# Optimization experiments

Measured on AMD Instinct MI355X. Metric: run time of the kernel, lower is better.

## Reference

```python
import jax, jax.numpy as jnp
import numpy as np
from jax.scipy.special import erf

L = 10          # grid_num_levels = int(log(8192/16)/log(2)) + 1
D = 4           # grid_level_dim
T = 1 << 21     # hash table size per level (2**log2_hashmap_size)
BASE = 16
RES = (BASE * (2 ** np.arange(L))).astype(np.float32)   # [16 .. 8192]
PRIMES = np.array([1, 2654435761, 805459861], dtype=np.uint32)
DIM_DIR_ENC = 3 + 2 * 3 * 4   # 27


def contract_mean_std(x, std):
    # mip-nerf-360 scene contraction + std scaled by |det J|^(1/3)
    r2 = jnp.maximum(jnp.sum(x * x, -1, keepdims=True), 1e-8)
    r = jnp.sqrt(r2)
    f = (2.0 * r - 1.0) / r2                  # tangential Jacobian eigenvalue
    z = jnp.where(r2 <= 1.0, x, f * x)
    det = (f * f) * (1.0 / r2)                # two tangential * one radial (1/r^2)
    scale = jnp.where(r2[..., 0] <= 1.0, 1.0, det[..., 0] ** (1.0 / 3.0))
    return z, std * scale


def pos_enc(x, min_deg=0, max_deg=4):
    scales = 2.0 ** jnp.arange(min_deg, max_deg, dtype=jnp.float32)
    xb = (x[..., None, :] * scales[:, None]).reshape(x.shape[:-1] + (-1,))
    four = jnp.sin(jnp.concatenate([xb, xb + 0.5 * jnp.pi], -1))
    return jnp.concatenate([x, four], -1)     # [..., 27]


def hash_grid_encode(x01, table):
    # x01: [..., 3] in [0,1]; table: [L, T, D] -> features [..., L, D]
    res = jnp.asarray(RES)
    primes = jnp.asarray(PRIMES)
    pos = x01[..., None, :] * res[:, None]    # [..., L, 3]
    pf = jnp.floor(pos)
    frac = pos - pf                           # differentiable w.r.t. pos
    base = pf.astype(jnp.uint32)
    lvl = jnp.arange(L)
    out = jnp.zeros(x01.shape[:-1] + (L, D), x01.dtype)
    for c in range(8):                        # fixed 8 trilinear corners
        off = np.array([(c >> 0) & 1, (c >> 1) & 1, (c >> 2) & 1], np.uint32)
        h = (base + off) * primes             # uint32 wraps = spatial hash
        idx = ((h[..., 0] ^ h[..., 1] ^ h[..., 2]) & jnp.uint32(T - 1)).astype(jnp.int32)
        w = jnp.prod(jnp.where(off.astype(bool), frac, 1.0 - frac), axis=-1)  # [..., L]
        out = out + w[..., None] * table[lvl, idx]   # irregular gather [..., L, D]
    return out


def reference(means, stds, viewdirs, table, W1, b1, W2, b2, Wd0, bd0, Wd1, bd1, Wrgb, brgb):
    # predict_density: warp_fn='contract', then bound=2 rescale
    m, s = contract_mean_std(means, stds)
    m, s = m / 2.0, s / 2.0
    x01 = (m + 1.0) / 2.0                     # encoder bound=1 -> [0,1]
    feats = hash_grid_encode(x01, table)      # [R, S, n, L, D]
    aw = erf(1.0 / jnp.sqrt(8.0 * (s[..., None] ** 2) * (jnp.asarray(RES) ** 2)))  # [R,S,n,L]
    feats = jnp.mean(feats * aw[..., None], axis=-3)        # mean over gaussian samples n
    feats = feats.reshape(feats.shape[:-2] + (L * D,))      # [R, S, 40]
    x = jax.nn.relu(feats @ W1 + b1) @ W2 + b2              # density MLP -> [R, S, 256]
    density = jax.nn.softplus(x[..., 0] - 1.0)              # density_bias = -1
    de = pos_enc(viewdirs)                                  # [R, 27]
    de = jnp.broadcast_to(de[..., None, :], x.shape[:-1] + (de.shape[-1],))
    inp = jnp.concatenate([x, de], -1)                      # [R, S, 283]
    y = jax.nn.relu(inp @ Wd0 + bd0)
    y = jnp.concatenate([y, inp], -1)                       # skip_layer_dir = 0
    y = jax.nn.relu(y @ Wd1 + bd1)
    rgb = jax.nn.sigmoid(y @ Wrgb + brgb)                   # premult=1, bias=0
    rgb = rgb * (1.0 + 2.0 * 0.001) - 0.001                 # rgb_padding
    return jnp.concatenate([density[..., None], rgb], -1)   # [R, S, 4] = (density, rgb)


def _linear(key, fan_in, fan_out):
    kw, kb = jax.random.split(key)
    s = 1.0 / np.sqrt(fan_in)
    W = jax.random.uniform(kw, (fan_in, fan_out), jnp.float32, -s, s)
    b = jax.random.uniform(kb, (fan_out,), jnp.float32, -s, s)
    return W, b


def setup_inputs() -> dict:
    key = jax.random.key(0)
    ks = jax.random.split(key, 10)
    R_, S_, n_ = 4096, 32, 6
    means = jax.random.normal(ks[0], (R_, S_, n_, 3), jnp.float32) * 1.5
    stds = jax.random.uniform(ks[1], (R_, S_, n_), jnp.float32) * 0.2 + 0.01
    vd = jax.random.normal(ks[2], (R_, 3), jnp.float32)
    viewdirs = vd / jnp.linalg.norm(vd, axis=-1, keepdims=True)
    table = jax.random.uniform(ks[3], (L, T, D), jnp.float32, -1e-4, 1e-4)
    W1, b1 = _linear(ks[4], L * D, 64)
    W2, b2 = _linear(ks[5], 64, 256)
    Wd0, bd0 = _linear(ks[6], 256 + DIM_DIR_ENC, 256)
    Wd1, bd1 = _linear(ks[7], 256 + 256 + DIM_DIR_ENC, 256)
    Wrgb, brgb = _linear(ks[8], 256, 3)
    return dict(means=means, stds=stds, viewdirs=viewdirs, table=table,
                W1=W1, b1=b1, W2=W2, b2=b2, Wd0=Wd0, bd0=bd0,
                Wd1=Wd1, bd1=bd1, Wrgb=Wrgb, brgb=brgb)
```

## Files before the change

kernel.cpp:

```cpp
#include <hip/hip_runtime.h>
#include <hip/hip_bf16.h>
#include <math.h>
#include <string.h>

#define NR 4096
#define NSMP 32
#define NG 6
#define NP (NR*NSMP)
#define NPS (NP*NG)
#define NL 10
#define TBL (1u<<21)
#define TMASK (TBL-1u)
#define PR1 2654435761u
#define PR2 805459861u

typedef __hip_bfloat16 bf16;
typedef __attribute__((ext_vector_type(8))) short short8;
typedef __attribute__((ext_vector_type(4))) float f32x4;

__device__ inline short f2bf_bits(float f) {
    __hip_bfloat16 h = __float2bfloat16(f);
    return (short)__builtin_bit_cast(unsigned short, h);
}

__global__ __launch_bounds__(256) void k_contract(const float* __restrict__ means,
                                                  const float* __restrict__ stds,
                                                  float4* __restrict__ ctr) {
    int i = blockIdx.x * 256 + threadIdx.x;
    if (i >= NPS) return;
    float x = means[i*3+0], y = means[i*3+1], z = means[i*3+2];
    float r2 = fmaxf(x*x + y*y + z*z, 1e-8f);
    float r  = sqrtf(r2);
    float f  = (2.f*r - 1.f) / r2;
    float zx, zy, zz, scale;
    if (r2 <= 1.f) { zx = x; zy = y; zz = z; scale = 1.f; }
    else { zx = f*x; zy = f*y; zz = f*z; scale = cbrtf(f*f / r2); }
    float s = stds[i] * scale * 0.5f;
    ctr[i] = make_float4(zx*0.25f + 0.5f, zy*0.25f + 0.5f, zz*0.25f + 0.5f, s);
}

__global__ __launch_bounds__(256) void k_encode(const float4* __restrict__ ctr,
                                                const float* __restrict__ table,
                                                float4* __restrict__ feats) {
    int p = blockIdx.x * 256 + threadIdx.x;
    int l = blockIdx.y;
    float res = (float)(16 << l);
    const float* tl = table + (size_t)l * TBL * 4u;
    float a0 = 0.f, a1 = 0.f, a2 = 0.f, a3 = 0.f;
    for (int s = 0; s < NG; s++) {
        float4 c = ctr[p*NG + s];
        float sr = c.w * res;
        float aw = erff(rsqrtf(8.f * sr * sr));
        float px = c.x*res, py = c.y*res, pz = c.z*res;
        float fx = floorf(px), fy = floorf(py), fz = floorf(pz);
        float rx = px - fx, ry = py - fy, rz = pz - fz;
        unsigned bx = (unsigned)fx, by = (unsigned)fy, bz = (unsigned)fz;
        unsigned hx[2] = { bx, bx + 1u };
        unsigned hy[2] = { by * PR1, (by + 1u) * PR1 };
        unsigned hz[2] = { bz * PR2, (bz + 1u) * PR2 };
        float wx[2] = { 1.f - rx, rx };
        float wy[2] = { 1.f - ry, ry };
        float wz[2] = { 1.f - rz, rz };
        #pragma unroll
        for (int cz = 0; cz < 2; cz++)
        #pragma unroll
        for (int cy = 0; cy < 2; cy++)
        #pragma unroll
        for (int cx = 0; cx < 2; cx++) {
            unsigned idx = (hx[cx] ^ hy[cy] ^ hz[cz]) & TMASK;
            float4 fv = *(const float4*)(tl + (size_t)idx * 4u);
            float w = wx[cx] * wy[cy] * wz[cz] * aw;
            a0 += w * fv.x; a1 += w * fv.y; a2 += w * fv.z; a3 += w * fv.w;
        }
    }
    const float inv = 1.f / 6.f;
    feats[(size_t)p * NL + l] = make_float4(a0*inv, a1*inv, a2*inv, a3*inv);
}

__global__ void k_dirs(const float* __restrict__ vd, float* __restrict__ de) {
    int r = blockIdx.x * 64 + threadIdx.x;
    if (r >= NR) return;
    float v0 = vd[r*3], v1 = vd[r*3+1], v2 = vd[r*3+2];
    float* o = de + r * 27;
    o[0] = v0; o[1] = v1; o[2] = v2;
    float v[3] = { v0, v1, v2 };
    #pragma unroll
    for (int sc = 0; sc < 4; sc++) {
        float scale = (float)(1 << sc);
        #pragma unroll
        for (int d = 0; d < 3; d++) {
            float xb = v[d] * scale;
            o[3  + sc*3 + d] = sinf(xb);
            o[15 + sc*3 + d] = cosf(xb);
        }
    }
}

__global__ __launch_bounds__(256) void k_l1(const float* __restrict__ Af,
                                            const float* __restrict__ W,
                                            const float* __restrict__ bias,
                                            bf16* __restrict__ Cout) {
    const int K = 40, N = 64;
    __shared__ float As[16][68];
    __shared__ float Ws[16][64];
    int tid = threadIdx.x;
    int tx = tid & 15, ty = tid >> 4;
    int m0 = blockIdx.x * 64;
    float acc[4][4] = {};
    for (int kb = 0; kb < K; kb += 16) {
        #pragma unroll
        for (int i = 0; i < 4; i++) {
            int idx = tid + i * 256;
            int kk = idx & 15, mm = idx >> 4;
            int k = kb + kk;
            As[kk][mm] = (k < K) ? Af[(size_t)(m0 + mm) * 40 + k] : 0.f;
        }
        #pragma unroll
        for (int i = 0; i < 4; i++) {
            int idx = tid + i * 256;
            int c = idx & 63, rr = idx >> 6;
            int k = kb + rr;
            Ws[rr][c] = (k < K) ? W[(size_t)k * N + c] : 0.f;
        }
        __syncthreads();
        #pragma unroll
        for (int kk = 0; kk < 16; kk++) {
            float4 a = *(const float4*)&As[kk][ty * 4];
            float4 b = *(const float4*)&Ws[kk][tx * 4];
            float av[4] = { a.x, a.y, a.z, a.w };
            float bv[4] = { b.x, b.y, b.z, b.w };
            #pragma unroll
            for (int i2 = 0; i2 < 4; i2++)
            #pragma unroll
            for (int j = 0; j < 4; j++)
                acc[i2][j] += av[i2] * bv[j];
        }
        __syncthreads();
    }
    #pragma unroll
    for (int i = 0; i < 4; i++) {
        int m = m0 + ty * 4 + i;
        #pragma unroll
        for (int j = 0; j < 4; j++) {
            int n = tx * 4 + j;
            float v = fmaxf(acc[i][j] + bias[n], 0.f);
            Cout[(size_t)m * N + n] = __float2bfloat16(v);
        }
    }
}

__global__ __launch_bounds__(256) void k_prepw(const float* __restrict__ W2,
                                               const float* __restrict__ Wd0,
                                               const float* __restrict__ Wd1,
                                               short* __restrict__ Wt2,
                                               short* __restrict__ Wt3,
                                               short* __restrict__ Wt4) {
    int i = blockIdx.x * 256 + threadIdx.x;
    if (i < 256*64) {
        int n = i >> 6, k = i & 63;
        Wt2[i] = f2bf_bits(W2[(size_t)k*256 + n]);
        return;
    }
    i -= 256*64;
    if (i < 256*320) {
        int n = i / 320, k = i % 320;
        Wt3[i] = f2bf_bits(k < 283 ? Wd0[(size_t)k*256 + n] : 0.f);
        return;
    }
    i -= 256*320;
    if (i < 256*576) {
        int n = i / 576, k = i % 576;
        Wt4[i] = f2bf_bits(k < 539 ? Wd1[(size_t)k*256 + n] : 0.f);
    }
}

template<int LAYER>
__device__ inline short8 load_chunk(const short* __restrict__ A0,
                                    const short* __restrict__ A1,
                                    const float* __restrict__ de,
                                    int m, int k) {
    if constexpr (LAYER == 2) {
        return *(const short8*)(A0 + (size_t)m * 64 + k);
    } else if constexpr (LAYER == 3) {
        if (k < 256) return *(const short8*)(A0 + (size_t)m * 256 + k);
        short8 v;
        int ray = m >> 5;
        #pragma unroll
        for (int j = 0; j < 8; j++) {
            int kk = k + j - 256;
            v[j] = f2bf_bits((kk < 27) ? de[ray * 27 + kk] : 0.f);
        }
        return v;
    } else {
        if (k < 256) return *(const short8*)(A0 + (size_t)m * 256 + k);
        if (k < 512) return *(const short8*)(A1 + (size_t)m * 256 + (k - 256));
        short8 v;
        int ray = m >> 5;
        #pragma unroll
        for (int j = 0; j < 8; j++) {
            int kk = k + j - 512;
            v[j] = f2bf_bits((kk < 27) ? de[ray * 27 + kk] : 0.f);
        }
        return v;
    }
}

template<int LAYER>
__global__ __launch_bounds__(256) void k_mlp(const short* __restrict__ A0,
                                             const short* __restrict__ A1,
                                             const float* __restrict__ de,
                                             const short* __restrict__ Wt,
                                             const float* __restrict__ bias,
                                             short* __restrict__ Cout,
                                             float* __restrict__ dens) {
    constexpr int KP = (LAYER == 2) ? 64 : (LAYER == 3) ? 320 : 576;
    __shared__ __align__(16) char As[8192];
    int tid = threadIdx.x;
    int wid = tid >> 6, lane = tid & 63;
    int m0 = blockIdx.x * 64;
    int l15 = lane & 15, l4 = lane >> 4;

    f32x4 acc[4][4] = {};
    for (int kt = 0; kt < KP / 64; kt++) {
        #pragma unroll
        for (int i = 0; i < 2; i++) {
            int q = tid + i * 256;
            int m = q >> 3, k8 = q & 7;
            short8 v = load_chunk<LAYER>(A0, A1, de, m0 + m, kt * 64 + k8 * 8);
            *(short8*)(As + ((m * 128 + k8 * 16) ^ ((m & 7) << 4))) = v;
        }
        __syncthreads();
        #pragma unroll
        for (int ks = 0; ks < 2; ks++) {
            short8 bfr[4], afr[4];
            #pragma unroll
            for (int nf = 0; nf < 4; nf++)
                bfr[nf] = *(const short8*)(Wt + (size_t)(wid * 64 + nf * 16 + l15) * KP
                                              + kt * 64 + ks * 32 + l4 * 8);
            #pragma unroll
            for (int mf = 0; mf < 4; mf++) {
                int m = mf * 16 + l15;
                afr[mf] = *(const short8*)(As + ((m * 128 + (ks * 4 + l4) * 16) ^ ((m & 7) << 4)));
            }
            #pragma unroll
            for (int mf = 0; mf < 4; mf++)
            #pragma unroll
            for (int nf = 0; nf < 4; nf++)
                acc[mf][nf] = __builtin_amdgcn_mfma_f32_16x16x32_bf16(afr[mf], bfr[nf], acc[mf][nf], 0, 0, 0);
        }
        __syncthreads();
    }

    #pragma unroll
    for (int mf = 0; mf < 4; mf++) {
        #pragma unroll
        for (int nf = 0; nf < 4; nf++) {
            int col = wid * 64 + nf * 16 + l15;
            float b = bias[col];
            #pragma unroll
            for (int r = 0; r < 4; r++) {
                int row = m0 + mf * 16 + l4 * 4 + r;
                float v = acc[mf][nf][r] + b;
                if constexpr (LAYER == 2) {
                    if (col == 0) {
                        float t = v - 1.f;
                        dens[(size_t)row * 4] = (t > 20.f) ? t : log1pf(expf(t));
                    }
                } else {
                    v = fmaxf(v, 0.f);
                }
                Cout[(size_t)row * 256 + col] = f2bf_bits(v);
            }
        }
    }
}

__global__ __launch_bounds__(256) void k_rgb(const short* __restrict__ y1,
                                             const float* __restrict__ Wrgb,
                                             const float* __restrict__ brgb,
                                             float* __restrict__ out) {
    typedef __attribute__((ext_vector_type(4))) short short4v;
    int lane = threadIdx.x & 63;
    int p = blockIdx.x * 4 + (threadIdx.x >> 6);
    short4v yv = *(const short4v*)(y1 + (size_t)p * 256 + lane * 4);
    float y[4];
    #pragma unroll
    for (int j = 0; j < 4; j++) {
        unsigned u = ((unsigned)(unsigned short)yv[j]) << 16;
        y[j] = __builtin_bit_cast(float, u);
    }
    float4 w0 = *(const float4*)(Wrgb + lane * 12);
    float4 w1 = *(const float4*)(Wrgb + lane * 12 + 4);
    float4 w2 = *(const float4*)(Wrgb + lane * 12 + 8);
    float wf[12] = { w0.x, w0.y, w0.z, w0.w, w1.x, w1.y, w1.z, w1.w, w2.x, w2.y, w2.z, w2.w };
    float a0 = 0.f, a1 = 0.f, a2 = 0.f;
    #pragma unroll
    for (int j = 0; j < 4; j++) {
        a0 += y[j] * wf[j*3 + 0];
        a1 += y[j] * wf[j*3 + 1];
        a2 += y[j] * wf[j*3 + 2];
    }
    #pragma unroll
    for (int off = 32; off > 0; off >>= 1) {
        a0 += __shfl_xor(a0, off);
        a1 += __shfl_xor(a1, off);
        a2 += __shfl_xor(a2, off);
    }
    if (lane == 0) {
        float s0 = 1.f / (1.f + expf(-(a0 + brgb[0])));
        float s1 = 1.f / (1.f + expf(-(a1 + brgb[1])));
        float s2 = 1.f / (1.f + expf(-(a2 + brgb[2])));
        out[(size_t)p * 4 + 1] = s0 * 1.002f - 0.001f;
        out[(size_t)p * 4 + 2] = s1 * 1.002f - 0.001f;
        out[(size_t)p * 4 + 3] = s2 * 1.002f - 0.001f;
    }
}

extern "C" void kernel_launch(void* const* d_in, const int* in_sizes, int n_in,
                              void* d_out, int out_size, void* d_ws, size_t ws_size,
                              hipStream_t stream) {
    const float* means = (const float*)d_in[0];
    const float* stds  = (const float*)d_in[1];
    const float* vd    = (const float*)d_in[2];
    const float* table = (const float*)d_in[3];
    const float* W1    = (const float*)d_in[4];
    const float* b1    = (const float*)d_in[5];
    const float* W2    = (const float*)d_in[6];
    const float* b2    = (const float*)d_in[7];
    const float* Wd0   = (const float*)d_in[8];
    const float* bd0   = (const float*)d_in[9];
    const float* Wd1   = (const float*)d_in[10];
    const float* bd1   = (const float*)d_in[11];
    const float* Wrgb  = (const float*)d_in[12];
    const float* brgb  = (const float*)d_in[13];
    float* out = (float*)d_out;

    char* ws = (char*)d_ws;
    float4* ctr   = (float4*)(ws);
    float4* feats = (float4*)(ws + 12582912);
    float*  de    = (float*) (ws + 33554432);
    short*  h1    = (short*) (ws + 33996800);
    short*  x     = (short*) (ws + 50774016);
    short*  y0    = (short*) (ws + 117882880);
    short*  y1    = (short*) (ws + 184991744);
    short*  Wt2   = (short*)(ws);
    short*  Wt3   = (short*)(ws + 32768);
    short*  Wt4   = (short*)(ws + 196608);

    k_contract<<<dim3(NPS/256), 256, 0, stream>>>(means, stds, ctr);
    k_encode<<<dim3(NP/256, NL), 256, 0, stream>>>(ctr, table, feats);
    k_dirs<<<dim3(NR/64), 64, 0, stream>>>(vd, de);
    k_prepw<<<dim3(960), 256, 0, stream>>>(W2, Wd0, Wd1, Wt2, Wt3, Wt4);
    k_l1<<<dim3(NP/64), 256, 0, stream>>>((const float*)feats, W1, b1, (bf16*)h1);
    k_mlp<2><<<dim3(NP/64), 256, 0, stream>>>(h1, nullptr, nullptr, Wt2, b2, x, out);
    k_mlp<3><<<dim3(NP/64), 256, 0, stream>>>(x, nullptr, de, Wt3, bd0, y0, nullptr);
    k_mlp<4><<<dim3(NP/64), 256, 0, stream>>>(y0, x, de, Wt4, bd1, y1, nullptr);
    k_rgb<<<dim3(NP/4), 256, 0, stream>>>(y1, Wrgb, brgb, out);
}
```

Measured before the change: 1.164 ms.

## Gather hash grid levels 3+ from a bf16 copy of the table

Adds a pre-pass that converts hash-table levels 3 through 9 to bf16 in workspace, then splits the encoder into a float path for coarse levels and a bf16 path for fine levels. The aim is to halve the bytes fetched per random corner gather and improve cache residency for the large levels. This adds a full-table conversion pass each call and reduces the precision of the table features; the sample loop is also unrolled.

Measured after the change: 1.147 ms. No clear change (-1.5%).

```diff
diff --git a/kernel.cpp b/kernel.cpp
--- a/kernel.cpp
+++ b/kernel.cpp
@@ -13,6 +13,8 @@
 #define TMASK (TBL-1u)
 #define PR1 2654435761u
 #define PR2 805459861u
+#define HLV0 3
+#define NHL (NL - HLV0)
 
 typedef __hip_bfloat16 bf16;
 typedef __attribute__((ext_vector_type(8))) short short8;
@@ -21,6 +23,9 @@
 __device__ inline short f2bf_bits(float f) {
     __hip_bfloat16 h = __float2bfloat16(f);
     return (short)__builtin_bit_cast(unsigned short, h);
+}
+__device__ inline float bfbits2f(unsigned short u) {
+    return __builtin_bit_cast(float, ((unsigned)u) << 16);
 }
 
 __global__ __launch_bounds__(256) void k_contract(const float* __restrict__ means,
@@ -39,14 +44,34 @@
     ctr[i] = make_float4(zx*0.25f + 0.5f, zy*0.25f + 0.5f, zz*0.25f + 0.5f, s);
 }
 
+__global__ __launch_bounds__(256) void k_prept(const float* __restrict__ table,
+                                               ushort4* __restrict__ th) {
+    size_t i = ((size_t)blockIdx.x * 256 + threadIdx.x) * 2;
+    const float4* src = (const float4*)(table + (size_t)HLV0 * TBL * 4u);
+    #pragma unroll
+    for (int j = 0; j < 2; j++) {
+        float4 v = src[i + j];
+        ushort4 o;
+        o.x = (unsigned short)f2bf_bits(v.x);
+        o.y = (unsigned short)f2bf_bits(v.y);
+        o.z = (unsigned short)f2bf_bits(v.z);
+        o.w = (unsigned short)f2bf_bits(v.w);
+        th[i + j] = o;
+    }
+}
+
+template<int BASE, bool HI>
 __global__ __launch_bounds__(256) void k_encode(const float4* __restrict__ ctr,
                                                 const float* __restrict__ table,
+                                                const ushort4* __restrict__ th,
                                                 float4* __restrict__ feats) {
     int p = blockIdx.x * 256 + threadIdx.x;
-    int l = blockIdx.y;
+    int l = BASE + blockIdx.y;
     float res = (float)(16 << l);
-    const float* tl = table + (size_t)l * TBL * 4u;
+    const float4* tf = (const float4*)(table + (size_t)l * TBL * 4u);
+    const ushort4* thl = th + (size_t)(l - HLV0) * TBL;
     float a0 = 0.f, a1 = 0.f, a2 = 0.f, a3 = 0.f;
+    #pragma unroll
     for (int s = 0; s < NG; s++) {
         float4 c = ctr[p*NG + s];
         float sr = c.w * res;
@@ -68,9 +93,17 @@
         #pragma unroll
         for (int cx = 0; cx < 2; cx++) {
             unsigned idx = (hx[cx] ^ hy[cy] ^ hz[cz]) & TMASK;
-            float4 fv = *(const float4*)(tl + (size_t)idx * 4u);
+            float v0, v1, v2, v3;
+            if constexpr (HI) {
+                ushort4 e = thl[idx];
+                v0 = bfbits2f(e.x); v1 = bfbits2f(e.y);
+                v2 = bfbits2f(e.z); v3 = bfbits2f(e.w);
+            } else {
+                float4 fv = tf[idx];
+                v0 = fv.x; v1 = fv.y; v2 = fv.z; v3 = fv.w;
+            }
             float w = wx[cx] * wy[cy] * wz[cz] * aw;
-            a0 += w * fv.x; a1 += w * fv.y; a2 += w * fv.z; a3 += w * fv.w;
+            a0 += w * v0; a1 += w * v1; a2 += w * v2; a3 += w * v3;
         }
     }
     const float inv = 1.f / 6.f;
@@ -346,9 +379,12 @@
     short*  Wt2   = (short*)(ws);
     short*  Wt3   = (short*)(ws + 32768);
     short*  Wt4   = (short*)(ws + 196608);
+    ushort4* tblH = (ushort4*)(ws + 50774016);
 
     k_contract<<<dim3(NPS/256), 256, 0, stream>>>(means, stds, ctr);
-    k_encode<<<dim3(NP/256, NL), 256, 0, stream>>>(ctr, table, feats);
+    k_prept<<<dim3(28672), 256, 0, stream>>>(table, tblH);
+    k_encode<0,false><<<dim3(NP/256, HLV0), 256, 0, stream>>>(ctr, table, tblH, feats);
+    k_encode<HLV0,true><<<dim3(NP/256, NHL), 256, 0, stream>>>(ctr, table, tblH, feats);
     k_dirs<<<dim3(NR/64), 64, 0, stream>>>(vd, de);
     k_prepw<<<dim3(960), 256, 0, stream>>>(W2, Wd0, Wd1, Wt2, Wt3, Wt4);
     k_l1<<<dim3(NP/64), 256, 0, stream>>>((const float*)feats, W1, b1, (bf16*)h1);
```
